# Kernel tuning notes

Hardware: AMD Instinct MI355X
Metric: run time of the kernel (lower is better)

The kernel has to match this reference:

```python
import jax, jax.numpy as jnp
import numpy as np
from jax import lax

N_GAUSS = 4096


def setup_inputs() -> dict:
    key = jax.random.key(0)
    k1, k2, k3, k4 = jax.random.split(key, 4)
    return {
        "_xyz": jax.random.normal(k1, (N_GAUSS, 3), dtype=jnp.float32),
        "_scaling": jax.random.normal(k2, (N_GAUSS, 3), dtype=jnp.float32),
        "_rotation": jax.random.normal(k3, (N_GAUSS, 4), dtype=jnp.float32),
        "_opacity": jax.random.normal(k4, (N_GAUSS, 1), dtype=jnp.float32),
        "resolution": 64,
        "num_blocks": 16,
    }


def _extract_fields(_xyz, _scaling, _rotation, _opacity, resolution, num_blocks):
    relax_ratio = 1.5
    block_size = 2.0 / num_blocks
    split_size = resolution // num_blocks

    # opacity activation + threshold mask (kept dense; masked gaussians get 0 weight)
    opacities = jax.nn.sigmoid(_opacity)[:, 0]  # [N]
    keep = opacities > 0.005
    opa = jnp.where(keep, opacities, 0.0)

    BIG = jnp.float32(1e10)
    mn = jnp.min(jnp.where(keep[:, None], _xyz, BIG), axis=0)
    mx = jnp.max(jnp.where(keep[:, None], _xyz, -BIG), axis=0)
    center = (mn + mx) / 2
    scale = 1.8 / jnp.max(mx - mn)
    xyzs = (_xyz - center) * scale           # [N,3] normalized positions
    stds = jnp.exp(_scaling) * scale         # [N,3] scaling activation * scale

    # covariance from scaling+rotation: L = R @ diag(s); C = L L^T
    q = _rotation / jnp.linalg.norm(_rotation, axis=1, keepdims=True)
    r, x, y, z = q[:, 0], q[:, 1], q[:, 2], q[:, 3]
    R = jnp.stack([
        jnp.stack([1 - 2 * (y * y + z * z), 2 * (x * y - r * z), 2 * (x * z + r * y)], -1),
        jnp.stack([2 * (x * y + r * z), 1 - 2 * (x * x + z * z), 2 * (y * z - r * x)], -1),
        jnp.stack([2 * (x * z - r * y), 2 * (y * z + r * x), 1 - 2 * (x * x + y * y)], -1),
    ], axis=1)                               # [N,3,3]
    L = R * stds[:, None, :]                 # R @ diag(s)
    C = jnp.einsum('nij,nkj->nik', L, L)     # [N,3,3]
    a, b, c = C[:, 0, 0], C[:, 0, 1], C[:, 0, 2]
    d, e, f = C[:, 1, 1], C[:, 1, 2], C[:, 2, 2]

    # analytic 3x3 symmetric inverse (precomputed per gaussian)
    inv_det = 1.0 / (a * d * f + 2 * e * c * b - e * e * a - c * c * d - b * b * f + 1e-24)
    inv_a = (d * f - e * e) * inv_det
    inv_b = (e * c - b * f) * inv_det
    inv_c = (e * b - c * d) * inv_det
    inv_d = (a * f - c * c) * inv_det
    inv_e = (b * c - e * a) * inv_det
    inv_f = (a * d - b * b) * inv_det

    lin = jnp.linspace(-1.0, 1.0, resolution).astype(jnp.float32)
    nb = num_blocks
    bi, bj, bk = jnp.meshgrid(jnp.arange(nb), jnp.arange(nb), jnp.arange(nb), indexing='ij')
    blocks = jnp.stack([bi.ravel(), bj.ravel(), bk.ravel()], axis=1)  # [nb^3, 3]
    off = jnp.arange(split_size)
    relax = block_size * relax_ratio

    def block_val(blk):
        xs = lin[blk[0] * split_size + off]
        ys = lin[blk[1] * split_size + off]
        zs = lin[blk[2] * split_size + off]
        xx, yy, zz = jnp.meshgrid(xs, ys, zs, indexing='ij')
        pts = jnp.stack([xx.ravel(), yy.ravel(), zz.ravel()], axis=-1)  # [S^3, 3]
        vmin = pts.min(0) - relax
        vmax = pts.max(0) + relax
        inside = jnp.all((xyzs < vmax) & (xyzs > vmin), axis=1)  # [N]
        w_opa = jnp.where(inside, opa, 0.0)                      # [N]
        dxyz = pts[:, None, :] - xyzs[None, :, :]                # [S^3, N, 3]
        px, py, pz = dxyz[..., 0], dxyz[..., 1], dxyz[..., 2]
        power = (-0.5 * (px * px * inv_a + py * py * inv_d + pz * pz * inv_f)
                 - px * py * inv_b - px * pz * inv_c - py * pz * inv_e)
        power = jnp.where(power > 0, jnp.float32(-1e10), power)
        val = jnp.sum(w_opa * jnp.exp(power), axis=1)            # [S^3]
        return val.reshape(split_size, split_size, split_size)

    vals = lax.map(block_val, blocks)  # [nb^3, S, S, S]
    occ = (vals.reshape(nb, nb, nb, split_size, split_size, split_size)
               .transpose(0, 3, 1, 4, 2, 5)
               .reshape(resolution, resolution, resolution))
    return occ


def reference(_xyz, _scaling, _rotation, _opacity, resolution, num_blocks):
    return _extract_fields(_xyz, _scaling, _rotation, _opacity, resolution, num_blocks)
```

## Files before the change

### kernel.cpp

```cpp
#include <hip/hip_runtime.h>

#define NG 4096
#define RELAX 0.1875f
#define KEEPTH -5.2933049f

__device__ __forceinline__ float linf(int i) { return -1.0f + (2.0f/63.0f)*(float)i; }
__device__ __forceinline__ int cperm(int i) { return (i & 1) ? 7 + ((i+1)>>1) : 7 - (i>>1); }

template<int T>
__device__ __forceinline__ float4 block_minmax_cs(
    const float4* __restrict__ xyz4, const float4* __restrict__ op4,
    int tid, float (*s_r)[6])
{
  float mn0=1e10f, mn1=1e10f, mn2=1e10f;
  float mx0=-1e10f, mx1=-1e10f, mx2=-1e10f;
  #pragma unroll
  for (int t = 0; t < NG/4/T; ++t) {
    const int G = t*T + tid;
    float4 v0 = xyz4[3*G+0], v1 = xyz4[3*G+1], v2 = xyz4[3*G+2];
    float4 oo = op4[G];
    if (oo.x > KEEPTH) { mn0=fminf(mn0,v0.x); mx0=fmaxf(mx0,v0.x);
                         mn1=fminf(mn1,v0.y); mx1=fmaxf(mx1,v0.y);
                         mn2=fminf(mn2,v0.z); mx2=fmaxf(mx2,v0.z); }
    if (oo.y > KEEPTH) { mn0=fminf(mn0,v0.w); mx0=fmaxf(mx0,v0.w);
                         mn1=fminf(mn1,v1.x); mx1=fmaxf(mx1,v1.x);
                         mn2=fminf(mn2,v1.y); mx2=fmaxf(mx2,v1.y); }
    if (oo.z > KEEPTH) { mn0=fminf(mn0,v1.z); mx0=fmaxf(mx0,v1.z);
                         mn1=fminf(mn1,v1.w); mx1=fmaxf(mx1,v1.w);
                         mn2=fminf(mn2,v2.x); mx2=fmaxf(mx2,v2.x); }
    if (oo.w > KEEPTH) { mn0=fminf(mn0,v2.y); mx0=fmaxf(mx0,v2.y);
                         mn1=fminf(mn1,v2.z); mx1=fmaxf(mx1,v2.z);
                         mn2=fminf(mn2,v2.w); mx2=fmaxf(mx2,v2.w); }
  }
  #pragma unroll
  for (int s = 1; s < 64; s <<= 1) {
    mn0 = fminf(mn0, __shfl_xor(mn0, s)); mx0 = fmaxf(mx0, __shfl_xor(mx0, s));
    mn1 = fminf(mn1, __shfl_xor(mn1, s)); mx1 = fmaxf(mx1, __shfl_xor(mx1, s));
    mn2 = fminf(mn2, __shfl_xor(mn2, s)); mx2 = fmaxf(mx2, __shfl_xor(mx2, s));
  }
  if ((tid & 63) == 0) {
    const int w = tid >> 6;
    s_r[w][0]=mn0; s_r[w][1]=mn1; s_r[w][2]=mn2;
    s_r[w][3]=mx0; s_r[w][4]=mx1; s_r[w][5]=mx2;
  }
  __syncthreads();
  mn0 = s_r[0][0]; mn1 = s_r[0][1]; mn2 = s_r[0][2];
  mx0 = s_r[0][3]; mx1 = s_r[0][4]; mx2 = s_r[0][5];
  #pragma unroll
  for (int w = 1; w < T/64; ++w) {
    mn0 = fminf(mn0, s_r[w][0]); mn1 = fminf(mn1, s_r[w][1]); mn2 = fminf(mn2, s_r[w][2]);
    mx0 = fmaxf(mx0, s_r[w][3]); mx1 = fmaxf(mx1, s_r[w][4]); mx2 = fmaxf(mx2, s_r[w][5]);
  }
  return make_float4((mn0+mx0)*0.5f, (mn1+mx1)*0.5f, (mn2+mx2)*0.5f,
                     1.8f/fmaxf(mx0-mn0, fmaxf(mx1-mn1, mx2-mn2)));
}

__device__ __forceinline__ void transform_one(
    const float* __restrict__ xyz, const float* __restrict__ scal,
    const float* __restrict__ rot, const float* __restrict__ opac,
    int g, float cx, float cy, float cz, float sc, float4* __restrict__ rec)
{
  float o = opac[g];
  float sig = 1.0f/(1.0f + __expf(-o));
  float opa = (sig > 0.005f) ? sig : 0.0f;
  float xs = (xyz[3*g+0]-cx)*sc;
  float ys = (xyz[3*g+1]-cy)*sc;
  float zs = (xyz[3*g+2]-cz)*sc;
  float sdx = __expf(scal[3*g+0])*sc;
  float sdy = __expf(scal[3*g+1])*sc;
  float sdz = __expf(scal[3*g+2])*sc;
  float qr=rot[4*g+0], qx=rot[4*g+1], qy=rot[4*g+2], qz=rot[4*g+3];
  float qn = 1.0f/sqrtf(qr*qr+qx*qx+qy*qy+qz*qz);
  qr*=qn; qx*=qn; qy*=qn; qz*=qn;
  float R00 = 1.0f-2.0f*(qy*qy+qz*qz), R01 = 2.0f*(qx*qy-qr*qz), R02 = 2.0f*(qx*qz+qr*qy);
  float R10 = 2.0f*(qx*qy+qr*qz), R11 = 1.0f-2.0f*(qx*qx+qz*qz), R12 = 2.0f*(qy*qz-qr*qx);
  float R20 = 2.0f*(qx*qz-qr*qy), R21 = 2.0f*(qy*qz+qr*qx), R22 = 1.0f-2.0f*(qx*qx+qy*qy);
  float L00=R00*sdx, L01=R01*sdy, L02=R02*sdz;
  float L10=R10*sdx, L11=R11*sdy, L12=R12*sdz;
  float L20=R20*sdx, L21=R21*sdy, L22=R22*sdz;
  float a = L00*L00+L01*L01+L02*L02;
  float bb= L00*L10+L01*L11+L02*L12;
  float cc= L00*L20+L01*L21+L02*L22;
  float d = L10*L10+L11*L11+L12*L12;
  float e = L10*L20+L11*L21+L12*L22;
  float f = L20*L20+L21*L21+L22*L22;
  float det = a*d*f + 2.0f*e*cc*bb - e*e*a - cc*cc*d - bb*bb*f + 1e-24f;
  float idt = 1.0f/det;
  float ia=(d*f-e*e)*idt, ib=(e*cc-bb*f)*idt, ic=(e*bb-cc*d)*idt;
  float id=(a*f-cc*cc)*idt, ie=(bb*cc-e*a)*idt, iff=(a*d-bb*bb)*idt;
  rec[3*g+0] = make_float4(xs, ys, zs, opa);
  rec[3*g+1] = make_float4(-0.5f*ia, -ib, -ic, -0.5f*id);
  rec[3*g+2] = make_float4(-ie, -0.5f*iff, 0.0f, 0.0f);
}

__global__ __launch_bounds__(256) void gm_prep(
    const float* __restrict__ xyz, const float* __restrict__ scal,
    const float* __restrict__ rot, const float* __restrict__ opac,
    float4* __restrict__ rec)
{
  __shared__ float s_r[8][6];
  const int tid = threadIdx.x;
  const int b   = blockIdx.x;
  const float4* xyz4 = (const float4*)xyz;
  const float4* op4  = (const float4*)opac;
  const float4 cs = block_minmax_cs<256>(xyz4, op4, tid, s_r);
  if (tid < 16)
    transform_one(xyz, scal, rot, opac, b*16+tid, cs.x, cs.y, cs.z, cs.w, rec);
}

__global__ __launch_bounds__(512) void gm_eval(
    const float4* __restrict__ rec, float* __restrict__ out)
{
  __shared__ float4 s_g[8][64*3];
  __shared__ float  s_p[8][64];
  const int tid  = threadIdx.x;
  const int w    = tid >> 6;
  const int lane = tid & 63;
  const int b = blockIdx.x;
  const int bi = cperm(b >> 8), bj = cperm((b >> 4) & 15), bk = cperm(b & 15);
  const float vminx = linf(bi*4) - RELAX, vmaxx = linf(bi*4+3) + RELAX;
  const float vminy = linf(bj*4) - RELAX, vmaxy = linf(bj*4+3) + RELAX;
  const float vminz = linf(bk*4) - RELAX, vmaxz = linf(bk*4+3) + RELAX;
  const int sx = lane >> 4, sy = (lane >> 2) & 3, sz = lane & 3;
  const float ptx = linf(bi*4+sx), pty = linf(bj*4+sy), ptz = linf(bk*4+sz);
  float acc = 0.0f;

  #pragma unroll
  for (int scn = 0; scn < 8; ++scn) {
    const int g = w*512 + scn*64 + lane;
    const float4 P = rec[3*g+0];
    const bool pass = (P.w > 0.0f &&
                       P.x > vminx && P.x < vmaxx &&
                       P.y > vminy && P.y < vmaxy &&
                       P.z > vminz && P.z < vmaxz);
    const unsigned long long mask = __ballot(pass);
    const int m = __popcll(mask);
    if (m == 0) continue;
    if (pass) {
      const int slot = __popcll(mask & ((1ull << lane) - 1ull));
      s_g[w][3*slot+0] = P;
      s_g[w][3*slot+1] = rec[3*g+1];
      s_g[w][3*slot+2] = rec[3*g+2];
    }
    __builtin_amdgcn_wave_barrier();
    for (int j = 0; j < m; ++j) {
      float4 Pq = s_g[w][3*j+0];
      float4 I0 = s_g[w][3*j+1];
      float4 I1 = s_g[w][3*j+2];
      float px = ptx - Pq.x, py = pty - Pq.y, pz = ptz - Pq.z;
      float power = px*px*I0.x + py*py*I0.w + pz*pz*I1.y
                  + px*py*I0.y + px*pz*I0.z + py*pz*I1.x;
      power = (power > 0.0f) ? -1e10f : power;
      acc += Pq.w * __expf(power);
    }
    __builtin_amdgcn_wave_barrier();
  }

  s_p[w][lane] = acc;
  __syncthreads();
  if (w == 0) {
    float v = 0.0f;
    #pragma unroll
    for (int q = 0; q < 8; ++q) v += s_p[q][lane];
    out[(bi*4+sx)*4096 + (bj*4+sy)*64 + (bk*4+sz)] = v;
  }
}

__global__ __launch_bounds__(256) void gm_fused_nows(
    const float* __restrict__ xyz, const float* __restrict__ scal,
    const float* __restrict__ rot, const float* __restrict__ opac,
    float* __restrict__ out)
{
  __shared__ float s_r[8][6];
  __shared__ float4 s_g[256*3];
  __shared__ float  s_acc[256];
  __shared__ int    s_cnt;
  const int tid = threadIdx.x;
  const float4* xyz4 = (const float4*)xyz;
  const float4* op4  = (const float4*)opac;
  if (tid == 0) s_cnt = 0;
  const float4 cs = block_minmax_cs<256>(xyz4, op4, tid, s_r);
  const float cx = cs.x, cy = cs.y, cz = cs.z, sc = cs.w;

  const int bin = blockIdx.x;
  const int bi = bin >> 8, bj = (bin >> 4) & 15, bk = bin & 15;
  const float vminx = linf(bi*4) - RELAX, vmaxx = linf(bi*4+3) + RELAX;
  const float vminy = linf(bj*4) - RELAX, vmaxy = linf(bj*4+3) + RELAX;
  const float vminz = linf(bk*4) - RELAX, vmaxz = linf(bk*4+3) + RELAX;
  const int p    = tid & 63;
  const int part = tid >> 6;
  const int sx = p >> 4, sy = (p >> 2) & 3, sz = p & 3;
  const float ptx = linf(bi*4+sx), pty = linf(bj*4+sy), ptz = linf(bk*4+sz);
  float acc = 0.0f;
  __syncthreads();

  for (int c0 = 0; c0 < NG; c0 += 256) {
    const int g = c0 + tid;
    float o = opac[g];
    bool pass = false;
    float xs=0, ys=0, zs=0, sig=0;
    if (o > KEEPTH) {
      sig = 1.0f/(1.0f + __expf(-o));
      xs = (xyz[3*g+0]-cx)*sc;
      ys = (xyz[3*g+1]-cy)*sc;
      zs = (xyz[3*g+2]-cz)*sc;
      pass = xs > vminx && xs < vmaxx &&
             ys > vminy && ys < vmaxy &&
             zs > vminz && zs < vmaxz;
    }
    if (pass) {
      float sdx = __expf(scal[3*g+0])*sc;
      float sdy = __expf(scal[3*g+1])*sc;
      float sdz = __expf(scal[3*g+2])*sc;
      float qr=rot[4*g+0], qx=rot[4*g+1], qy=rot[4*g+2], qz=rot[4*g+3];
      float qn = 1.0f/sqrtf(qr*qr+qx*qx+qy*qy+qz*qz);
      qr*=qn; qx*=qn; qy*=qn; qz*=qn;
      float R00 = 1.0f-2.0f*(qy*qy+qz*qz), R01 = 2.0f*(qx*qy-qr*qz), R02 = 2.0f*(qx*qz+qr*qy);
      float R10 = 2.0f*(qx*qy+qr*qz), R11 = 1.0f-2.0f*(qx*qx+qz*qz), R12 = 2.0f*(qy*qz-qr*qx);
      float R20 = 2.0f*(qx*qz-qr*qy), R21 = 2.0f*(qy*qz+qr*qx), R22 = 1.0f-2.0f*(qx*qx+qy*qy);
      float L00=R00*sdx, L01=R01*sdy, L02=R02*sdz;
      float L10=R10*sdx, L11=R11*sdy, L12=R12*sdz;
      float L20=R20*sdx, L21=R21*sdy, L22=R22*sdz;
      float a = L00*L00+L01*L01+L02*L02;
      float bb= L00*L10+L01*L11+L02*L12;
      float cc= L00*L20+L01*L21+L02*L22;
      float d = L10*L10+L11*L11+L12*L12;
      float e = L10*L20+L11*L21+L12*L22;
      float f = L20*L20+L21*L21+L22*L22;
      float det = a*d*f + 2.0f*e*cc*bb - e*e*a - cc*cc*d - bb*bb*f + 1e-24f;
      float idt = 1.0f/det;
      float ia=(d*f-e*e)*idt, ib=(e*cc-bb*f)*idt, ic=(e*bb-cc*d)*idt;
      float id=(a*f-cc*cc)*idt, ie=(bb*cc-e*a)*idt, iff=(a*d-bb*bb)*idt;
      int slot = atomicAdd(&s_cnt, 1);
      s_g[3*slot+0] = make_float4(xs, ys, zs, sig);
      s_g[3*slot+1] = make_float4(-0.5f*ia, -ib, -ic, -0.5f*id);
      s_g[3*slot+2] = make_float4(-ie, -0.5f*iff, 0.0f, 0.0f);
    }
    __syncthreads();
    const int nn = s_cnt;
    #pragma unroll 4
    for (int j = part; j < nn; j += 4) {
      float4 P  = s_g[3*j+0];
      float4 I0 = s_g[3*j+1];
      float4 I1 = s_g[3*j+2];
      float px = ptx - P.x, py = pty - P.y, pz = ptz - P.z;
      float power = px*px*I0.x + py*py*I0.w + pz*pz*I1.y
                  + px*py*I0.y + px*pz*I0.z + py*pz*I1.x;
      power = (power > 0.0f) ? -1e10f : power;
      acc += P.w * __expf(power);
    }
    __syncthreads();
    if (tid == 0) s_cnt = 0;
    __syncthreads();
  }
  s_acc[tid] = acc;
  __syncthreads();
  if (tid < 64) {
    float v = s_acc[tid] + s_acc[tid+64] + s_acc[tid+128] + s_acc[tid+192];
    out[(bi*4+sx)*4096 + (bj*4+sy)*64 + (bk*4+sz)] = v;
  }
}

extern "C" void kernel_launch(void* const* d_in, const int* in_sizes, int n_in,
                              void* d_out, int out_size, void* d_ws, size_t ws_size,
                              hipStream_t stream) {
  const float* xyz  = (const float*)d_in[0];
  const float* scal = (const float*)d_in[1];
  const float* rot  = (const float*)d_in[2];
  const float* opac = (const float*)d_in[3];
  float* out = (float*)d_out;
  float4* rec = (float4*)d_ws;

  if (ws_size >= 196608) {
    gm_prep<<<256, 256, 0, stream>>>(xyz, scal, rot, opac, rec);
    gm_eval<<<4096, 512, 0, stream>>>(rec, out);
  } else {
    gm_fused_nows<<<4096, 256, 0, stream>>>(xyz, scal, rot, opac, out);
  }
}
```

Baseline: 121.9 us.

## Split gaussian records into SoA pos/inv arrays and prefetch next positions

Splits the 48-byte per-gaussian workspace record into a contiguous position array and a separate inverse-covariance array, so the culling scan in the eval kernel reads dense 16-byte entries instead of strided ones. The eval loop now software-prefetches the next chunk's positions while testing the current chunk, which hides global load latency behind the ballot and compaction work. The prep kernel moves to 512 threads for its min/max reduction. The cost is slightly more register pressure from the prefetch and a split workspace layout.

After: 112.0 us. -8.2%, faster.

```diff
diff --git a/kernel.cpp b/kernel.cpp
--- a/kernel.cpp
+++ b/kernel.cpp
@@ -58,7 +58,8 @@
 __device__ __forceinline__ void transform_one(
     const float* __restrict__ xyz, const float* __restrict__ scal,
     const float* __restrict__ rot, const float* __restrict__ opac,
-    int g, float cx, float cy, float cz, float sc, float4* __restrict__ rec)
+    int g, float cx, float cy, float cz, float sc,
+    float4* __restrict__ pos, float4* __restrict__ inv)
 {
   float o = opac[g];
   float sig = 1.0f/(1.0f + __expf(-o));
@@ -88,28 +89,29 @@
   float idt = 1.0f/det;
   float ia=(d*f-e*e)*idt, ib=(e*cc-bb*f)*idt, ic=(e*bb-cc*d)*idt;
   float id=(a*f-cc*cc)*idt, ie=(bb*cc-e*a)*idt, iff=(a*d-bb*bb)*idt;
-  rec[3*g+0] = make_float4(xs, ys, zs, opa);
-  rec[3*g+1] = make_float4(-0.5f*ia, -ib, -ic, -0.5f*id);
-  rec[3*g+2] = make_float4(-ie, -0.5f*iff, 0.0f, 0.0f);
-}
-
-__global__ __launch_bounds__(256) void gm_prep(
+  pos[g]     = make_float4(xs, ys, zs, opa);
+  inv[2*g+0] = make_float4(-0.5f*ia, -ib, -ic, -0.5f*id);
+  inv[2*g+1] = make_float4(-ie, -0.5f*iff, 0.0f, 0.0f);
+}
+
+__global__ __launch_bounds__(512) void gm_prep(
     const float* __restrict__ xyz, const float* __restrict__ scal,
     const float* __restrict__ rot, const float* __restrict__ opac,
-    float4* __restrict__ rec)
+    float4* __restrict__ pos, float4* __restrict__ inv)
 {
   __shared__ float s_r[8][6];
   const int tid = threadIdx.x;
   const int b   = blockIdx.x;
   const float4* xyz4 = (const float4*)xyz;
   const float4* op4  = (const float4*)opac;
-  const float4 cs = block_minmax_cs<256>(xyz4, op4, tid, s_r);
+  const float4 cs = block_minmax_cs<512>(xyz4, op4, tid, s_r);
   if (tid < 16)
-    transform_one(xyz, scal, rot, opac, b*16+tid, cs.x, cs.y, cs.z, cs.w, rec);
+    transform_one(xyz, scal, rot, opac, b*16+tid, cs.x, cs.y, cs.z, cs.w, pos, inv);
 }
 
 __global__ __launch_bounds__(512) void gm_eval(
-    const float4* __restrict__ rec, float* __restrict__ out)
+    const float4* __restrict__ pos, const float4* __restrict__ inv,
+    float* __restrict__ out)
 {
   __shared__ float4 s_g[8][64*3];
   __shared__ float  s_p[8][64];
@@ -123,37 +125,42 @@
   const float vminz = linf(bk*4) - RELAX, vmaxz = linf(bk*4+3) + RELAX;
   const int sx = lane >> 4, sy = (lane >> 2) & 3, sz = lane & 3;
   const float ptx = linf(bi*4+sx), pty = linf(bj*4+sy), ptz = linf(bk*4+sz);
+  const int gbase = w*512 + lane;
   float acc = 0.0f;
 
+  float4 P = pos[gbase];
   #pragma unroll
   for (int scn = 0; scn < 8; ++scn) {
-    const int g = w*512 + scn*64 + lane;
-    const float4 P = rec[3*g+0];
+    const int g = gbase + scn*64;
+    float4 Pn;
+    if (scn < 7) Pn = pos[g + 64];
     const bool pass = (P.w > 0.0f &&
                        P.x > vminx && P.x < vmaxx &&
                        P.y > vminy && P.y < vmaxy &&
                        P.z > vminz && P.z < vmaxz);
     const unsigned long long mask = __ballot(pass);
     const int m = __popcll(mask);
-    if (m == 0) continue;
-    if (pass) {
-      const int slot = __popcll(mask & ((1ull << lane) - 1ull));
-      s_g[w][3*slot+0] = P;
-      s_g[w][3*slot+1] = rec[3*g+1];
-      s_g[w][3*slot+2] = rec[3*g+2];
-    }
-    __builtin_amdgcn_wave_barrier();
-    for (int j = 0; j < m; ++j) {
-      float4 Pq = s_g[w][3*j+0];
-      float4 I0 = s_g[w][3*j+1];
-      float4 I1 = s_g[w][3*j+2];
-      float px = ptx - Pq.x, py = pty - Pq.y, pz = ptz - Pq.z;
-      float power = px*px*I0.x + py*py*I0.w + pz*pz*I1.y
-                  + px*py*I0.y + px*pz*I0.z + py*pz*I1.x;
-      power = (power > 0.0f) ? -1e10f : power;
-      acc += Pq.w * __expf(power);
-    }
-    __builtin_amdgcn_wave_barrier();
+    if (m != 0) {
+      if (pass) {
+        const int slot = __popcll(mask & ((1ull << lane) - 1ull));
+        s_g[w][3*slot+0] = P;
+        s_g[w][3*slot+1] = inv[2*g+0];
+        s_g[w][3*slot+2] = inv[2*g+1];
+      }
+      __builtin_amdgcn_wave_barrier();
+      for (int j = 0; j < m; ++j) {
+        float4 Pq = s_g[w][3*j+0];
+        float4 I0 = s_g[w][3*j+1];
+        float4 I1 = s_g[w][3*j+2];
+        float px = ptx - Pq.x, py = pty - Pq.y, pz = ptz - Pq.z;
+        float power = px*px*I0.x + py*py*I0.w + pz*pz*I1.y
+                    + px*py*I0.y + px*pz*I0.z + py*pz*I1.x;
+        power = (power > 0.0f) ? -1e10f : power;
+        acc += Pq.w * __expf(power);
+      }
+      __builtin_amdgcn_wave_barrier();
+    }
+    P = Pn;
   }
 
   s_p[w][lane] = acc;
@@ -269,11 +276,13 @@
   const float* rot  = (const float*)d_in[2];
   const float* opac = (const float*)d_in[3];
   float* out = (float*)d_out;
-  float4* rec = (float4*)d_ws;
+  char* ws = (char*)d_ws;
+  float4* pos = (float4*)ws;
+  float4* inv = (float4*)(ws + 65536);
 
   if (ws_size >= 196608) {
-    gm_prep<<<256, 256, 0, stream>>>(xyz, scal, rot, opac, rec);
-    gm_eval<<<4096, 512, 0, stream>>>(rec, out);
+    gm_prep<<<256, 512, 0, stream>>>(xyz, scal, rot, opac, pos, inv);
+    gm_eval<<<4096, 512, 0, stream>>>(pos, inv, out);
   } else {
     gm_fused_nows<<<4096, 256, 0, stream>>>(xyz, scal, rot, opac, out);
   }
```
